# Performance work log

Measured on AMD Instinct MI355X. Metric: run time of the kernel, lower is better.

## Reference

```python
import jax, jax.numpy as jnp
import numpy as np


def setup_inputs() -> dict:
    key = jax.random.key(0)
    ks = jax.random.split(key, 6)
    B, N, F, H, E = 2, 50000, 64, 32, 800000
    x = jax.random.normal(ks[0], (B, N, F), dtype=jnp.float32)
    edge_index = jax.random.randint(ks[1], (2, E), 0, N, dtype=jnp.int64)
    h_cur = jax.random.normal(ks[2], (B, N, H), dtype=jnp.float32)
    c_cur = jax.random.normal(ks[3], (B, N, H), dtype=jnp.float32)
    W = jax.random.normal(ks[4], (F + H, 4 * H), dtype=jnp.float32) * (1.0 / np.sqrt(F + H))
    b = jax.random.normal(ks[5], (4 * H,), dtype=jnp.float32) * 0.01
    return {"x": x, "edge_index": edge_index, "h_cur": h_cur, "c_cur": c_cur, "W": W, "b": b}


def reference(x, edge_index, h_cur, c_cur, W, b):
    B, N, _ = x.shape
    H = h_cur.shape[-1]

    # --- GCNConv on concatenated [x, h] ---
    combined = jnp.concatenate([x, h_cur], axis=-1)          # [B, N, F+H]
    xw = jnp.einsum('bnf,fg->bng', combined, W)              # [B, N, 4H]

    # add self-loops
    loop = jnp.arange(N, dtype=edge_index.dtype)
    src = jnp.concatenate([edge_index[0], loop])             # [E+N]
    dst = jnp.concatenate([edge_index[1], loop])             # [E+N]

    # symmetric degree normalization: deg over target index (PyG gcn_norm)
    deg = jnp.zeros((N,), dtype=xw.dtype).at[dst].add(1.0)
    dinv = jnp.where(deg > 0, jax.lax.rsqrt(deg), 0.0)
    norm = dinv[src] * dinv[dst]                             # [E+N]

    # gather-scale-scatter aggregation
    msgs = xw[:, src, :] * norm[None, :, None]               # [B, E+N, 4H]
    agg = jnp.zeros((B, N, 4 * H), dtype=xw.dtype).at[:, dst, :].add(msgs)
    conv = agg + b                                           # [B, N, 4H]

    # --- LSTM gating ---
    cc_i, cc_f, cc_o, cc_g = jnp.split(conv, 4, axis=-1)
    i = jax.nn.sigmoid(cc_i)
    f = jax.nn.sigmoid(cc_f)
    o = jax.nn.sigmoid(cc_o)
    g = jnp.tanh(cc_g)
    c_next = f * c_cur + i * g
    h_next = o * jnp.tanh(c_next)
    return h_next, c_next
```

## Files before the change

### kernel.cpp

```cpp
#include <hip/hip_runtime.h>
#include <hip/hip_bf16.h>

constexpr int H_DIM = 32;
constexpr int KPAD  = 104;
constexpr int CAP   = 64;
constexpr int CHK   = 64;
constexpr int EPB   = 2048;

typedef __attribute__((ext_vector_type(8))) short bf16x8;
typedef __attribute__((ext_vector_type(4))) float f32x4;

static __device__ __forceinline__ unsigned short f2bf_bits(float v) {
    __hip_bfloat16 b = __float2bfloat16(v);
    return *reinterpret_cast<unsigned short*>(&b);
}
static __device__ __forceinline__ unsigned pack2(float a, float b) {
    return (unsigned)f2bf_bits(a) | ((unsigned)f2bf_bits(b) << 16);
}
static __device__ __forceinline__ float lo_f(unsigned u) { return __uint_as_float(u << 16); }
static __device__ __forceinline__ float hi_f(unsigned u) { return __uint_as_float(u & 0xffff0000u); }

static __device__ __forceinline__ void fma3p(const uint3 u, float d, float* a)
{
    a[0] = fmaf(lo_f(u.x), d, a[0]);
    a[3] = fmaf(hi_f(u.x), d, a[3]);
    a[1] = fmaf(lo_f(u.y), d, a[1]);
    a[4] = fmaf(hi_f(u.y), d, a[4]);
    a[2] = fmaf(lo_f(u.z), d, a[2]);
    a[5] = fmaf(hi_f(u.z), d, a[5]);
}

__global__ __launch_bounds__(256)
void part_convert_kernel(const float* __restrict__ x,
                         const float* __restrict__ h,
                         const int* __restrict__ ei,
                         unsigned* __restrict__ part_buf,
                         unsigned char* __restrict__ hcnt,
                         unsigned* __restrict__ z,
                         int N, int E, int NB)
{
    const int bi = blockIdx.x;
    const int t  = threadIdx.x;
    if (bi < NB) {
        __shared__ unsigned loff[256];
        loff[t] = 0u;
        __syncthreads();
        const int e0 = bi * EPB + t;
        #pragma unroll
        for (int j = 0; j < 8; ++j) {
            int e = e0 + 256 * j;
            if (e < E) {
                int src = ei[e];
                int dst = ei[E + e];
                int p   = dst >> 8;
                unsigned pos = atomicAdd(&loff[p], 1u);
                if (pos < CHK)
                    part_buf[((long)p * NB + bi) * CHK + pos] =
                        (unsigned)src | ((unsigned)(dst & 255) << 16);
            }
        }
        __syncthreads();
        hcnt[bi * 256 + t] = (unsigned char)min(loff[t], (unsigned)CHK);
        return;
    }

    long idx = (long)(bi - NB) * 256 + t;
    if (idx >= (long)N * 24) return;
    int n  = (int)(idx / 24);
    int ku = (int)(idx - (long)n * 24);
    int f0 = 4 * ku;
    float4 a, b;
    if (f0 < 64) {
        a = *reinterpret_cast<const float4*>(x + (long)n * 64 + f0);
        b = *reinterpret_cast<const float4*>(x + ((long)N + n) * 64 + f0);
    } else {
        a = *reinterpret_cast<const float4*>(h + (long)n * 32 + (f0 - 64));
        b = *reinterpret_cast<const float4*>(h + ((long)N + n) * 32 + (f0 - 64));
    }
    uint4 o;
    o.x = pack2(a.x, b.x);
    o.y = pack2(a.y, b.y);
    o.z = pack2(a.z, b.z);
    o.w = pack2(a.w, b.w);
    *reinterpret_cast<uint4*>(z + idx * 4) = o;
}

__global__ __launch_bounds__(256)
void bucket_prep_kernel(const unsigned* __restrict__ part_buf,
                        const unsigned char* __restrict__ hcnt,
                        const float* __restrict__ W,
                        unsigned short* __restrict__ Wt,
                        unsigned* __restrict__ cnt,
                        unsigned short* __restrict__ bucket,
                        int N, int NB, int NPART)
{
    const int t = threadIdx.x;
    if ((int)blockIdx.x >= NPART) {
        int gt = ((int)blockIdx.x - NPART) * 256 + t;
        if (gt < 96 * 128) {
            int k = gt >> 7;
            int n = gt & 127;
            Wt[n * 96 + k] = f2bf_bits(W[gt]);
        }
        return;
    }

    __shared__ unsigned lcnt[256];
    __shared__ __align__(16) unsigned short lbuck[256 * CAP];
    const int p = blockIdx.x;
    lcnt[t] = 0u;
    __syncthreads();

    for (int c = t; c < NB; c += 256) {
        int cc = (int)hcnt[c * 256 + p];
        const unsigned* __restrict__ pb = part_buf + ((long)p * NB + c) * CHK;
        for (int jj = 0; jj < cc; jj += 4) {
            uint4 u4 = *reinterpret_cast<const uint4*>(pb + jj);
            unsigned uu[4] = {u4.x, u4.y, u4.z, u4.w};
            #pragma unroll
            for (int q2 = 0; q2 < 4; ++q2) {
                if (jj + q2 < cc) {
                    unsigned u = uu[q2];
                    int dl = (int)((u >> 16) & 0xFFu);
                    unsigned pos = atomicAdd(&lcnt[dl], 1u);
                    if (pos < CAP) lbuck[dl * CAP + pos] = (unsigned short)(u & 0xFFFFu);
                }
            }
        }
    }
    __syncthreads();

    int n = p * 256 + t;
    if (n < N) cnt[n] = lcnt[t];
    #pragma unroll
    for (int j = 0; j < 8; ++j) {
        int idx = t + 256 * j;
        int row = idx >> 3, c = idx & 7;
        int nn = p * 256 + row;
        if (nn < N)
            *reinterpret_cast<uint4*>(bucket + (long)nn * CAP + 8 * c) =
                *reinterpret_cast<const uint4*>(&lbuck[row * CAP + 8 * c]);
    }
}

__global__ __launch_bounds__(256)
void gather_kernel(const unsigned* __restrict__ cnt,
                   const unsigned short* __restrict__ bucket,
                   const unsigned* __restrict__ z,
                   unsigned* __restrict__ aggz, int N)
{
    const int wid  = (int)(((long)blockIdx.x * 256 + threadIdx.x) >> 6);
    const int lane = threadIdx.x & 63;
    const int g    = lane >> 5;
    const int w    = lane & 31;
    const bool live = (wid < N);
    const int n = live ? wid : 0;

    const int dn = live ? min((int)cnt[n], CAP) : 0;
    const unsigned short* __restrict__ brow = bucket + (long)n * CAP;
    const unsigned* __restrict__ zw = z + 3 * w;

    float acc[6];
    #pragma unroll
    for (int j = 0; j < 6; ++j) acc[j] = 0.f;

    for (int base = 0; base < dn; base += 64) {
        int cnt64 = min(64, dn - base);
        int   s_reg = 0;
        float d_reg = 0.f;
        if (lane < cnt64) {
            s_reg = (int)brow[base + lane];
            d_reg = rsqrtf((float)cnt[s_reg] + 1.f);
        }
        for (int i = 0; i < cnt64; i += 16) {
            unsigned so[8]; float dd[8]; uint3 u[8];
            #pragma unroll
            for (int j = 0; j < 8; ++j) {
                int ij = i + 2 * j + g;
                so[j] = (unsigned)__shfl(s_reg, ij) * 96u;
                dd[j] = __shfl(d_reg, ij);
                if (ij >= cnt64) dd[j] = 0.f;
            }
            #pragma unroll
            for (int j = 0; j < 8; ++j) {
                int ij = i + 2 * j + g;
                u[j] = make_uint3(0u, 0u, 0u);
                if (ij < cnt64)
                    u[j] = *reinterpret_cast<const uint3*>(zw + so[j]);
            }
            #pragma unroll
            for (int j = 0; j < 8; ++j) fma3p(u[j], dd[j], acc);
        }
    }

    #pragma unroll
    for (int j = 0; j < 6; ++j) acc[j] += __shfl_xor(acc[j], 32);

    if (live && g == 0) {
        float di  = rsqrtf((float)cnt[n] + 1.f);
        float di2 = di * di;
        uint3 us = *reinterpret_cast<const uint3*>(zw + (unsigned)n * 96u);
        uint3 o;
        o.x = pack2(fmaf(di, acc[0], di2 * lo_f(us.x)), fmaf(di, acc[3], di2 * hi_f(us.x)));
        o.y = pack2(fmaf(di, acc[1], di2 * lo_f(us.y)), fmaf(di, acc[4], di2 * hi_f(us.y)));
        o.z = pack2(fmaf(di, acc[2], di2 * lo_f(us.z)), fmaf(di, acc[5], di2 * hi_f(us.z)));
        *reinterpret_cast<uint3*>(aggz + (unsigned)n * 96u + 3 * w) = o;
    }
}

__global__ __launch_bounds__(256)
void gemm_gates_kernel(const unsigned* __restrict__ aggz,
                       const unsigned short* __restrict__ Wt,
                       const float* __restrict__ bias,
                       const float* __restrict__ c_cur,
                       float* __restrict__ out,
                       int N)
{
    __shared__ __align__(16) unsigned short As[64 * KPAD];
    const int t  = threadIdx.x;
    const int n0 = blockIdx.x * 32;

    #pragma unroll
    for (int j = 0; j < 3; ++j) {
        int idx = t + 256 * j;
        int i   = idx / 24;
        int ku  = idx - 24 * i;
        int n   = n0 + i;
        uint4 u = make_uint4(0,0,0,0);
        if (n < N) u = *reinterpret_cast<const uint4*>(aggz + (long)n * 96 + 4 * ku);
        ushort4 lo, hi;
        lo.x = (unsigned short)u.x;  hi.x = (unsigned short)(u.x >> 16);
        lo.y = (unsigned short)u.y;  hi.y = (unsigned short)(u.y >> 16);
        lo.z = (unsigned short)u.z;  hi.z = (unsigned short)(u.z >> 16);
        lo.w = (unsigned short)u.w;  hi.w = (unsigned short)(u.w >> 16);
        *reinterpret_cast<ushort4*>(&As[i * KPAD + 4 * ku])        = lo;
        *reinterpret_cast<ushort4*>(&As[(32 + i) * KPAD + 4 * ku]) = hi;
    }
    __syncthreads();

    const int wv   = t >> 6;
    const int lane = t & 63;
    const int m    = lane & 15;
    const int q    = lane >> 4;

    f32x4 acc[8] = {};
    #pragma unroll
    for (int k0 = 0; k0 < 96; k0 += 32) {
        bf16x8 a = *reinterpret_cast<const bf16x8*>(&As[(wv * 16 + m) * KPAD + k0 + q * 8]);
        #pragma unroll
        for (int nt = 0; nt < 8; ++nt) {
            bf16x8 b = *reinterpret_cast<const bf16x8*>(&Wt[(nt * 16 + m) * 96 + k0 + q * 8]);
            acc[nt] = __builtin_amdgcn_mfma_f32_16x16x32_bf16(a, b, acc[nt], 0, 0, 0);
        }
    }

    const float bi0 = bias[m],       bi1 = bias[16 + m];
    const float bf0 = bias[32 + m],  bf1 = bias[48 + m];
    const float bo0 = bias[64 + m],  bo1 = bias[80 + m];
    const float bg0 = bias[96 + m],  bg1 = bias[112 + m];
    const long  co  = (long)2 * N * H_DIM;

    #pragma unroll
    for (int r = 0; r < 4; ++r) {
        int rr = wv * 16 + q * 4 + r;
        int b  = rr >> 5;
        int i  = rr & 31;
        int n  = n0 + i;
        if (n < N) {
            long base = ((long)b * N + n) * H_DIM;
            float c0 = c_cur[base + m];
            float c1 = c_cur[base + 16 + m];
            float ig0 = 1.f / (1.f + __expf(-(acc[0][r] + bi0)));
            float ig1 = 1.f / (1.f + __expf(-(acc[1][r] + bi1)));
            float fg0 = 1.f / (1.f + __expf(-(acc[2][r] + bf0)));
            float fg1 = 1.f / (1.f + __expf(-(acc[3][r] + bf1)));
            float og0 = 1.f / (1.f + __expf(-(acc[4][r] + bo0)));
            float og1 = 1.f / (1.f + __expf(-(acc[5][r] + bo1)));
            float gg0 = tanhf(acc[6][r] + bg0);
            float gg1 = tanhf(acc[7][r] + bg1);
            float cn0 = fmaf(fg0, c0, ig0 * gg0);
            float cn1 = fmaf(fg1, c1, ig1 * gg1);
            out[base + m]           = og0 * tanhf(cn0);
            out[base + 16 + m]      = og1 * tanhf(cn1);
            out[co + base + m]      = cn0;
            out[co + base + 16 + m] = cn1;
        }
    }
}

extern "C" void kernel_launch(void* const* d_in, const int* in_sizes, int n_in,
                              void* d_out, int out_size, void* d_ws, size_t ws_size,
                              hipStream_t stream)
{
    const float* x    = (const float*)d_in[0];
    const int*   ei   = (const int*)d_in[1];
    const float* h    = (const float*)d_in[2];
    const float* c    = (const float*)d_in[3];
    const float* W    = (const float*)d_in[4];
    const float* bias = (const float*)d_in[5];

    const int  E  = in_sizes[1] / 2;
    const long BN = (long)in_sizes[2] / H_DIM;
    const int  N  = (int)(BN / 2);
    const int  NP = (N + 255) >> 8;
    const int  NB = (E + EPB - 1) / EPB;

    char* ws = (char*)d_ws;
    unsigned* z = (unsigned*)ws;
    size_t off = (size_t)N * 96 * sizeof(unsigned);
    unsigned* aggz = (unsigned*)(ws + off);  off += (size_t)N * 96 * sizeof(unsigned);
    unsigned* cnt  = (unsigned*)(ws + off);  off += (size_t)N * sizeof(unsigned);
    unsigned short* bucket = (unsigned short*)(ws + off); off += (size_t)N * CAP * sizeof(unsigned short);
    unsigned short* Wt = (unsigned short*)(ws + off);     off += 96 * 128 * sizeof(unsigned short);
    off = (off + 255) & ~(size_t)255;
    unsigned* part_buf = (unsigned*)(ws + off); off += (size_t)NP * NB * CHK * sizeof(unsigned);
    unsigned char* hcnt = (unsigned char*)(ws + off); off += (size_t)NB * 256;

    int convGrid = (int)(((long)N * 24 + 255) / 256);
    part_convert_kernel<<<NB + convGrid, 256, 0, stream>>>(
        x, h, ei, part_buf, hcnt, z, N, E, NB);

    bucket_prep_kernel<<<NP + 48, 256, 0, stream>>>(
        part_buf, hcnt, W, Wt, cnt, bucket, N, NB, NP);

    int gGrid = (int)(((long)N * 64 + 255) / 256);
    gather_kernel<<<gGrid, 256, 0, stream>>>(cnt, bucket, z, aggz, N);

    int mGrid = (N + 31) / 32;
    gemm_gates_kernel<<<mGrid, 256, 0, stream>>>(aggz, Wt, bias, c, (float*)d_out, N);
}
```

Before: 189.1 us.

## Split gather into three feature-slice passes, two nodes per wavefront

Replaces the single gather kernel with three launches, each covering one 32-word (128-byte) slice of the 96-word bf16 feature row. Each wavefront now handles two destination nodes at once. The aim is to shrink the working set of z touched per pass so it stays in cache better, and to give each wave more independent loads in flight. The cost is reading the bucket and cnt arrays three times, launching three kernels instead of one, and narrower 4-byte loads in place of 12-byte loads.

```diff
diff --git a/kernel.cpp b/kernel.cpp
--- a/kernel.cpp
+++ b/kernel.cpp
@@ -19,16 +19,6 @@
 }
 static __device__ __forceinline__ float lo_f(unsigned u) { return __uint_as_float(u << 16); }
 static __device__ __forceinline__ float hi_f(unsigned u) { return __uint_as_float(u & 0xffff0000u); }
-
-static __device__ __forceinline__ void fma3p(const uint3 u, float d, float* a)
-{
-    a[0] = fmaf(lo_f(u.x), d, a[0]);
-    a[3] = fmaf(hi_f(u.x), d, a[3]);
-    a[1] = fmaf(lo_f(u.y), d, a[1]);
-    a[4] = fmaf(hi_f(u.y), d, a[4]);
-    a[2] = fmaf(lo_f(u.z), d, a[2]);
-    a[5] = fmaf(hi_f(u.z), d, a[5]);
-}
 
 __global__ __launch_bounds__(256)
 void part_convert_kernel(const float* __restrict__ x,
@@ -144,67 +134,77 @@
 }
 
 __global__ __launch_bounds__(256)
-void gather_kernel(const unsigned* __restrict__ cnt,
-                   const unsigned short* __restrict__ bucket,
-                   const unsigned* __restrict__ z,
-                   unsigned* __restrict__ aggz, int N)
+void gather_pass_kernel(const unsigned* __restrict__ cnt,
+                        const unsigned short* __restrict__ bucket,
+                        const unsigned* __restrict__ z,
+                        unsigned* __restrict__ aggz, int N, int pass)
 {
     const int wid  = (int)(((long)blockIdx.x * 256 + threadIdx.x) >> 6);
     const int lane = threadIdx.x & 63;
     const int g    = lane >> 5;
     const int w    = lane & 31;
-    const bool live = (wid < N);
-    const int n = live ? wid : 0;
-
-    const int dn = live ? min((int)cnt[n], CAP) : 0;
-    const unsigned short* __restrict__ brow = bucket + (long)n * CAP;
-    const unsigned* __restrict__ zw = z + 3 * w;
-
-    float acc[6];
-    #pragma unroll
-    for (int j = 0; j < 6; ++j) acc[j] = 0.f;
-
-    for (int base = 0; base < dn; base += 64) {
-        int cnt64 = min(64, dn - base);
-        int   s_reg = 0;
-        float d_reg = 0.f;
-        if (lane < cnt64) {
-            s_reg = (int)brow[base + lane];
-            d_reg = rsqrtf((float)cnt[s_reg] + 1.f);
-        }
-        for (int i = 0; i < cnt64; i += 16) {
-            unsigned so[8]; float dd[8]; uint3 u[8];
+    const int nA   = 2 * wid;
+    const int nB   = 2 * wid + 1;
+    const bool liveA = (nA < N), liveB = (nB < N);
+    const int naA = liveA ? nA : 0, naB = liveB ? nB : 0;
+    const int dnA = liveA ? min((int)cnt[naA], CAP) : 0;
+    const int dnB = liveB ? min((int)cnt[naB], CAP) : 0;
+    const unsigned short* __restrict__ browA = bucket + (long)naA * CAP;
+    const unsigned short* __restrict__ browB = bucket + (long)naB * CAP;
+    const unsigned* __restrict__ zw = z + 32 * pass + w;
+
+    float aA0 = 0.f, aA1 = 0.f, aB0 = 0.f, aB1 = 0.f;
+    const int dnM = max(dnA, dnB);
+    for (int base = 0; base < dnM; base += 64) {
+        int cA = min(64, max(0, dnA - base));
+        int cB = min(64, max(0, dnB - base));
+        int sA = 0, sB = 0; float dA = 0.f, dB = 0.f;
+        if (lane < cA) { sA = (int)browA[base + lane]; dA = rsqrtf((float)cnt[sA] + 1.f); }
+        if (lane < cB) { sB = (int)browB[base + lane]; dB = rsqrtf((float)cnt[sB] + 1.f); }
+        int cM = max(cA, cB);
+        for (int i = 0; i < cM; i += 16) {
+            unsigned soA[8], soB[8]; float ddA[8], ddB[8]; unsigned uA[8], uB[8];
             #pragma unroll
             for (int j = 0; j < 8; ++j) {
                 int ij = i + 2 * j + g;
-                so[j] = (unsigned)__shfl(s_reg, ij) * 96u;
-                dd[j] = __shfl(d_reg, ij);
-                if (ij >= cnt64) dd[j] = 0.f;
+                soA[j] = (unsigned)__shfl(sA, ij) * 96u;
+                ddA[j] = __shfl(dA, ij);  if (ij >= cA) ddA[j] = 0.f;
+                soB[j] = (unsigned)__shfl(sB, ij) * 96u;
+                ddB[j] = __shfl(dB, ij);  if (ij >= cB) ddB[j] = 0.f;
             }
             #pragma unroll
             for (int j = 0; j < 8; ++j) {
                 int ij = i + 2 * j + g;
-                u[j] = make_uint3(0u, 0u, 0u);
-                if (ij < cnt64)
-                    u[j] = *reinterpret_cast<const uint3*>(zw + so[j]);
+                uA[j] = 0u; uB[j] = 0u;
+                if (ij < cA) uA[j] = zw[soA[j]];
+                if (ij < cB) uB[j] = zw[soB[j]];
             }
             #pragma unroll
-            for (int j = 0; j < 8; ++j) fma3p(u[j], dd[j], acc);
-        }
-    }
-
-    #pragma unroll
-    for (int j = 0; j < 6; ++j) acc[j] += __shfl_xor(acc[j], 32);
-
-    if (live && g == 0) {
-        float di  = rsqrtf((float)cnt[n] + 1.f);
-        float di2 = di * di;
-        uint3 us = *reinterpret_cast<const uint3*>(zw + (unsigned)n * 96u);
-        uint3 o;
-        o.x = pack2(fmaf(di, acc[0], di2 * lo_f(us.x)), fmaf(di, acc[3], di2 * hi_f(us.x)));
-        o.y = pack2(fmaf(di, acc[1], di2 * lo_f(us.y)), fmaf(di, acc[4], di2 * hi_f(us.y)));
-        o.z = pack2(fmaf(di, acc[2], di2 * lo_f(us.z)), fmaf(di, acc[5], di2 * hi_f(us.z)));
-        *reinterpret_cast<uint3*>(aggz + (unsigned)n * 96u + 3 * w) = o;
+            for (int j = 0; j < 8; ++j) {
+                aA0 = fmaf(lo_f(uA[j]), ddA[j], aA0);
+                aA1 = fmaf(hi_f(uA[j]), ddA[j], aA1);
+                aB0 = fmaf(lo_f(uB[j]), ddB[j], aB0);
+                aB1 = fmaf(hi_f(uB[j]), ddB[j], aB1);
+            }
+        }
+    }
+
+    aA0 += __shfl_xor(aA0, 32);  aA1 += __shfl_xor(aA1, 32);
+    aB0 += __shfl_xor(aB0, 32);  aB1 += __shfl_xor(aB1, 32);
+
+    if (g == 0) {
+        if (liveA) {
+            float di = rsqrtf((float)cnt[naA] + 1.f), di2 = di * di;
+            unsigned us = zw[(unsigned)naA * 96u];
+            aggz[(unsigned)naA * 96u + 32 * pass + w] =
+                pack2(fmaf(di, aA0, di2 * lo_f(us)), fmaf(di, aA1, di2 * hi_f(us)));
+        }
+        if (liveB) {
+            float di = rsqrtf((float)cnt[naB] + 1.f), di2 = di * di;
+            unsigned us = zw[(unsigned)naB * 96u];
+            aggz[(unsigned)naB * 96u + 32 * pass + w] =
+                pack2(fmaf(di, aB0, di2 * lo_f(us)), fmaf(di, aB1, di2 * hi_f(us)));
+        }
     }
 }
 
@@ -323,8 +323,9 @@
     bucket_prep_kernel<<<NP + 48, 256, 0, stream>>>(
         part_buf, hcnt, W, Wt, cnt, bucket, N, NB, NP);
 
-    int gGrid = (int)(((long)N * 64 + 255) / 256);
-    gather_kernel<<<gGrid, 256, 0, stream>>>(cnt, bucket, z, aggz, N);
+    int gGrid = (int)((((long)((N + 1) / 2)) * 64 + 255) / 256);
+    for (int pass = 0; pass < 3; ++pass)
+        gather_pass_kernel<<<gGrid, 256, 0, stream>>>(cnt, bucket, z, aggz, N, pass);
 
     int mGrid = (N + 31) / 32;
     gemm_gates_kernel<<<mGrid, 256, 0, stream>>>(aggz, Wt, bias, c, (float*)d_out, N);
```

New measurement: 221.7 us. 1.17x slower.
